# Optimization experiments

Measured on AMD Instinct MI355X. Metric: run time of the kernel, lower is better.

## Reference

```python
import jax, jax.numpy as jnp
import numpy as np

M = 0.4
S = 64.0
EPS = 1e-5

def _normalize(x, axis=-1):
    n = jnp.linalg.norm(x, axis=axis, keepdims=True)
    return x / jnp.maximum(n, EPS)

def setup_inputs() -> dict:
    key = jax.random.key(0)
    k1, k2, k3 = jax.random.split(key, 3)
    B, D, C = 512, 512, 100000
    inp = jax.random.normal(k1, (B, D), dtype=jnp.float32)
    weight = jax.random.normal(k2, (C, D), dtype=jnp.float32) * (D ** -0.5)
    label = jax.random.randint(k3, (B,), 0, C, dtype=jnp.int64)
    bias = jnp.full((1,), float(np.log(C * 10)), dtype=jnp.float32)
    return {"input": inp, "label": label, "weight": weight, "bias": bias}

def reference(input, label, weight, bias):
    # cos_theta: [B, C]
    cos_theta = _normalize(input) @ _normalize(weight).T
    cos_m_theta_p = S * (cos_theta - M) - bias
    cos_m_theta_n = S * cos_theta - bias
    # log(1 + exp(x)) with clamp to [-S, S] as in the original
    p_loss = jnp.log1p(jnp.exp(-jnp.clip(cos_m_theta_p, -S, S)))
    n_loss = jnp.log1p(jnp.exp(jnp.clip(cos_m_theta_n, -S, S)))
    one_hot = jax.nn.one_hot(label, cos_theta.shape[1], dtype=jnp.bool_)
    losses = jnp.where(one_hot, p_loss, n_loss)
    return losses.sum(axis=1).mean()
```

## Files before the change

### kernel.cpp

```cpp
#include <hip/hip_runtime.h>
#include <hip/hip_bf16.h>
#include <stdint.h>

#define C_CLS  100000
#define DDIM   512
#define BROWS  512
#define NT     64
#define KC     32
#define NSTEP  (DDIM / KC)
#define EPSN   1e-5f

typedef __attribute__((ext_vector_type(8))) short short8;
typedef __attribute__((ext_vector_type(4))) float f32x4;

__device__ inline unsigned f2bf(float f) {
  unsigned u = __float_as_uint(f);
  u += 0x7fffu + ((u >> 16) & 1u);
  return u >> 16;
}

__global__ void k_zero(float* acc) { *acc = 0.f; }

__global__ void __launch_bounds__(64) k_norm_input(const float* __restrict__ in,
                                                   uint4* __restrict__ xnf) {
  int b = blockIdx.x;
  int lane = threadIdx.x;
  const float4* row = (const float4*)(in + b * DDIM);
  float4 v0 = row[lane * 2];
  float4 v1 = row[lane * 2 + 1];
  float ss = v0.x*v0.x + v0.y*v0.y + v0.z*v0.z + v0.w*v0.w
           + v1.x*v1.x + v1.y*v1.y + v1.z*v1.z + v1.w*v1.w;
#pragma unroll
  for (int o = 32; o >= 1; o >>= 1) ss += __shfl_xor(ss, o, 64);
  float sc = 1.f / fmaxf(sqrtf(ss), EPSN);
  uint4 o4;
  o4.x = f2bf(v0.x*sc) | (f2bf(v0.y*sc) << 16);
  o4.y = f2bf(v0.z*sc) | (f2bf(v0.w*sc) << 16);
  o4.z = f2bf(v1.x*sc) | (f2bf(v1.y*sc) << 16);
  o4.w = f2bf(v1.z*sc) | (f2bf(v1.w*sc) << 16);
  int idx = ((b >> 4) * 16 + (lane >> 2)) * 64 + (lane & 3) * 16 + (b & 15);
  xnf[idx] = o4;
}

__global__ void __launch_bounds__(512, 4) k_gemm(const uint4* __restrict__ xnf,
                                                 const float* __restrict__ wt,
                                                 const float* __restrict__ bias,
                                                 float* __restrict__ acc_out) {
  __shared__ __align__(16) unsigned char sW[4][4096];
  __shared__ float sNsq[NT];
  __shared__ float sRed[8];

  const int tid  = threadIdx.x;
  const int lane = tid & 63;
  const int wv   = tid >> 6;
  const int cbase = blockIdx.x * NT;

  const int cls = tid >> 3;
  const int q   = tid & 7;
  int wcls = cbase + cls;
  if (wcls >= C_CLS) wcls = C_CLS - 1;
  const float4* wsrc = (const float4*)(wt + (size_t)wcls * DDIM) + q;
  const int wbyte = ((cls >> 4) * 64 + (q >> 1) * 16 + (cls & 15)) * 16 + (q & 1) * 8;

  float wsq = 0.f;
  f32x4 acc[4][4];
#pragma unroll
  for (int m = 0; m < 4; m++)
#pragma unroll
    for (int n = 0; n < 4; n++) acc[m][n] = (f32x4)(0.f);

  auto cvt_write = [&](const float4& w, int bufi) {
    wsq += w.x*w.x + w.y*w.y + w.z*w.z + w.w*w.w;
    uint2 d;
    d.x = f2bf(w.x) | (f2bf(w.y) << 16);
    d.y = f2bf(w.z) | (f2bf(w.w) << 16);
    *(uint2*)(&sW[bufi][wbyte]) = d;
  };
  auto barrier = [&]() {
    __builtin_amdgcn_sched_barrier(0);
    asm volatile("s_waitcnt lgkmcnt(0)" ::: "memory");
    __builtin_amdgcn_s_barrier();
    __builtin_amdgcn_sched_barrier(0);
  };
  auto do_step = [&](int s, float4& wcur, float4& wnext) {
    short8 af[4];
#pragma unroll
    for (int m = 0; m < 4; m++) {
      int idx = ((wv * 4 + m) * 16 + s) * 64 + lane;
      af[m] = *(const short8*)&xnf[idx];
    }
    if (s + 2 < NSTEP) wnext = wsrc[(s + 2) * 8];
    if (s + 1 < NSTEP) cvt_write(wcur, (s + 1) & 3);
    barrier();
    const unsigned char* Wb = sW[s & 3];
#pragma unroll
    for (int n = 0; n < 4; n++) {
      short8 wf = *(const short8*)(Wb + (n * 64 + lane) * 16);
#pragma unroll
      for (int m = 0; m < 4; m++)
        acc[m][n] = __builtin_amdgcn_mfma_f32_16x16x32_bf16(af[m], wf, acc[m][n], 0, 0, 0);
    }
  };

  float4 wA = wsrc[0];
  float4 wB = wsrc[8];
  cvt_write(wA, 0);
  barrier();

#pragma unroll 1
  for (int s = 0; s < NSTEP; s += 2) {
    do_step(s,     wB, wA);
    do_step(s + 1, wA, wB);
  }

#pragma unroll
  for (int o = 1; o < 8; o <<= 1) wsq += __shfl_xor(wsq, o, 64);
  if ((tid & 7) == 0) sNsq[cls] = wsq;
  __syncthreads();

  const float bv = bias[0];
  float sum = 0.f;
#pragma unroll
  for (int n = 0; n < 4; n++) {
    int cl = n * 16 + (lane & 15);
    float rn = 1.f / fmaxf(sqrtf(sNsq[cl]), EPSN);
    bool valid = (cbase + cl) < C_CLS;
#pragma unroll
    for (int m = 0; m < 4; m++) {
#pragma unroll
      for (int i = 0; i < 4; i++) {
        float cosv = acc[m][n][i] * rn;
        float x = fminf(fmaf(cosv, 64.f, -bv), 64.f);
        float z = __expf(x);
        float l = z * fmaf(z, fmaf(z, 0.33333333f, -0.5f), 1.f);
        if (z > 0.03125f) l = __logf(1.f + z);
        sum += valid ? l : 0.f;
      }
    }
  }
#pragma unroll
  for (int o = 32; o >= 1; o >>= 1) sum += __shfl_xor(sum, o, 64);
  if (lane == 0) sRed[wv] = sum;
  __syncthreads();
  if (tid == 0) {
    float t = 0.f;
#pragma unroll
    for (int i = 0; i < 8; i++) t += sRed[i];
    atomicAdd(acc_out, t);
  }
}

__global__ void __launch_bounds__(64) k_label(const float* __restrict__ in,
                                              const float* __restrict__ wt,
                                              const int* __restrict__ label,
                                              const float* __restrict__ bias,
                                              float* __restrict__ acc_out) {
  int b = blockIdx.x;
  int lane = threadIdx.x;
  int c = label[b];
  const float4* xr = (const float4*)(in + b * DDIM);
  const float4* wr = (const float4*)(wt + (size_t)c * DDIM);
  float dt = 0.f, sx = 0.f, sw = 0.f;
#pragma unroll
  for (int i = 0; i < 2; i++) {
    float4 x = xr[lane * 2 + i];
    float4 w = wr[lane * 2 + i];
    dt += x.x*w.x + x.y*w.y + x.z*w.z + x.w*w.w;
    sx += x.x*x.x + x.y*x.y + x.z*x.z + x.w*x.w;
    sw += w.x*w.x + w.y*w.y + w.z*w.z + w.w*w.w;
  }
#pragma unroll
  for (int o = 32; o >= 1; o >>= 1) {
    dt += __shfl_xor(dt, o, 64);
    sx += __shfl_xor(sx, o, 64);
    sw += __shfl_xor(sw, o, 64);
  }
  if (lane == 0) {
    float bv = bias[0];
    float cosv = dt / (fmaxf(sqrtf(sx), EPSN) * fmaxf(sqrtf(sw), EPSN));
    float cp = 64.f * (cosv - 0.4f) - bv;
    cp = fminf(fmaxf(cp, -64.f), 64.f);
    float pl = log1pf(expf(-cp));
    float cn = 64.f * cosv - bv;
    cn = fminf(fmaxf(cn, -64.f), 64.f);
    float nl = log1pf(expf(cn));
    atomicAdd(acc_out, pl - nl);
  }
}

__global__ void k_final(const float* acc, float* out) { out[0] = acc[0] * (1.f / 512.f); }

extern "C" void kernel_launch(void* const* d_in, const int* in_sizes, int n_in,
                              void* d_out, int out_size, void* d_ws, size_t ws_size,
                              hipStream_t stream) {
  const float* input  = (const float*)d_in[0];
  const int*   label  = (const int*)d_in[1];
  const float* weight = (const float*)d_in[2];
  const float* bias   = (const float*)d_in[3];

  float* acc = (float*)d_ws;
  uint4* xnf = (uint4*)((char*)d_ws + 256);

  k_zero<<<1, 1, 0, stream>>>(acc);
  k_norm_input<<<BROWS, 64, 0, stream>>>(input, xnf);
  k_gemm<<<(C_CLS + NT - 1) / NT, 512, 0, stream>>>(xnf, weight, bias, acc);
  k_label<<<BROWS, 64, 0, stream>>>(input, weight, label, bias, acc);
  k_final<<<1, 1, 0, stream>>>(acc, (float*)d_out);
}
```

Before: 116.1 us.

## Restructure GEMM pipeline with prefetched A fragments, swizzled LDS, fewer launches

The main GEMM loop is restructured so the next step's A fragments and the W tile for three steps ahead are prefetched, with the barrier moved to the end of each step and the loop fully unrolled. Shared-memory W writes and reads get an XOR swizzle to reduce bank conflicts, and the normalized-input layout is reordered so A loads become contiguous per step. The zero and final kernels are removed by zeroing the output inside the norm kernel and scaling each atomic contribution by 1/512. bf16 packing now uses the HIP intrinsic. The extra prefetch buffers raise register pressure under launch bounds of 512 threads with 4 blocks.

```diff
diff --git a/kernel.cpp b/kernel.cpp
--- a/kernel.cpp
+++ b/kernel.cpp
@@ -6,25 +6,23 @@
 #define DDIM   512
 #define BROWS  512
 #define NT     64
-#define KC     32
-#define NSTEP  (DDIM / KC)
+#define NSTEP  16
 #define EPSN   1e-5f
 
 typedef __attribute__((ext_vector_type(8))) short short8;
 typedef __attribute__((ext_vector_type(4))) float f32x4;
 
-__device__ inline unsigned f2bf(float f) {
-  unsigned u = __float_as_uint(f);
-  u += 0x7fffu + ((u >> 16) & 1u);
-  return u >> 16;
-}
-
-__global__ void k_zero(float* acc) { *acc = 0.f; }
+__device__ inline unsigned pk2(float a, float b) {
+  __hip_bfloat162 h = __float22bfloat162_rn(make_float2(a, b));
+  unsigned u; __builtin_memcpy(&u, &h, 4); return u;
+}
 
 __global__ void __launch_bounds__(64) k_norm_input(const float* __restrict__ in,
-                                                   uint4* __restrict__ xnf) {
+                                                   uint4* __restrict__ xnf,
+                                                   float* __restrict__ out) {
   int b = blockIdx.x;
   int lane = threadIdx.x;
+  if (b == 0 && lane == 0) out[0] = 0.f;
   const float4* row = (const float4*)(in + b * DDIM);
   float4 v0 = row[lane * 2];
   float4 v1 = row[lane * 2 + 1];
@@ -34,18 +32,18 @@
   for (int o = 32; o >= 1; o >>= 1) ss += __shfl_xor(ss, o, 64);
   float sc = 1.f / fmaxf(sqrtf(ss), EPSN);
   uint4 o4;
-  o4.x = f2bf(v0.x*sc) | (f2bf(v0.y*sc) << 16);
-  o4.y = f2bf(v0.z*sc) | (f2bf(v0.w*sc) << 16);
-  o4.z = f2bf(v1.x*sc) | (f2bf(v1.y*sc) << 16);
-  o4.w = f2bf(v1.z*sc) | (f2bf(v1.w*sc) << 16);
-  int idx = ((b >> 4) * 16 + (lane >> 2)) * 64 + (lane & 3) * 16 + (b & 15);
+  o4.x = pk2(v0.x*sc, v0.y*sc);
+  o4.y = pk2(v0.z*sc, v0.w*sc);
+  o4.z = pk2(v1.x*sc, v1.y*sc);
+  o4.w = pk2(v1.z*sc, v1.w*sc);
+  int idx = ((lane >> 2) * 32 + (b >> 4)) * 64 + (lane & 3) * 16 + (b & 15);
   xnf[idx] = o4;
 }
 
 __global__ void __launch_bounds__(512, 4) k_gemm(const uint4* __restrict__ xnf,
                                                  const float* __restrict__ wt,
                                                  const float* __restrict__ bias,
-                                                 float* __restrict__ acc_out) {
+                                                 float* __restrict__ out) {
   __shared__ __align__(16) unsigned char sW[4][4096];
   __shared__ float sNsq[NT];
   __shared__ float sRed[8];
@@ -60,7 +58,11 @@
   int wcls = cbase + cls;
   if (wcls >= C_CLS) wcls = C_CLS - 1;
   const float4* wsrc = (const float4*)(wt + (size_t)wcls * DDIM) + q;
-  const int wbyte = ((cls >> 4) * 64 + (q >> 1) * 16 + (cls & 15)) * 16 + (q & 1) * 8;
+  const int wcell = (cls >> 4) * 64 + (q >> 1) * 16 + (cls & 15);
+  const int wbyte = ((wcell * 16) ^ (((wcell >> 4) & 3) << 4)) + (q & 1) * 8;
+  const int rbyte = (lane * 16) ^ (((lane >> 4) & 3) << 4);
+
+  const uint4* abase = xnf + wv * 256 + lane;
 
   float wsq = 0.f;
   f32x4 acc[4][4];
@@ -69,11 +71,16 @@
 #pragma unroll
     for (int n = 0; n < 4; n++) acc[m][n] = (f32x4)(0.f);
 
+  auto loadA = [&](short8* af, int s) {
+#pragma unroll
+    for (int m = 0; m < 4; m++)
+      af[m] = *(const short8*)(abase + s * 2048 + m * 64);
+  };
   auto cvt_write = [&](const float4& w, int bufi) {
     wsq += w.x*w.x + w.y*w.y + w.z*w.z + w.w*w.w;
     uint2 d;
-    d.x = f2bf(w.x) | (f2bf(w.y) << 16);
-    d.y = f2bf(w.z) | (f2bf(w.w) << 16);
+    d.x = pk2(w.x, w.y);
+    d.y = pk2(w.z, w.w);
     *(uint2*)(&sW[bufi][wbyte]) = d;
   };
   auto barrier = [&]() {
@@ -82,35 +89,33 @@
     __builtin_amdgcn_s_barrier();
     __builtin_amdgcn_sched_barrier(0);
   };
-  auto do_step = [&](int s, float4& wcur, float4& wnext) {
-    short8 af[4];
-#pragma unroll
-    for (int m = 0; m < 4; m++) {
-      int idx = ((wv * 4 + m) * 16 + s) * 64 + lane;
-      af[m] = *(const short8*)&xnf[idx];
+  auto step = [&](int s, float4& wreg, short8* afc, short8* afn) {
+    if (s + 1 < NSTEP) loadA(afn, s + 1);
+    if (s + 1 < NSTEP) cvt_write(wreg, (s + 1) & 3);
+    if (s + 3 < NSTEP) wreg = wsrc[(s + 3) * 8];
+    const unsigned char* Wb = sW[s & 3];
+#pragma unroll
+    for (int n = 0; n < 4; n++) {
+      short8 wf = *(const short8*)(Wb + n * 1024 + rbyte);
+#pragma unroll
+      for (int m = 0; m < 4; m++)
+        acc[m][n] = __builtin_amdgcn_mfma_f32_16x16x32_bf16(afc[m], wf, acc[m][n], 0, 0, 0);
     }
-    if (s + 2 < NSTEP) wnext = wsrc[(s + 2) * 8];
-    if (s + 1 < NSTEP) cvt_write(wcur, (s + 1) & 3);
-    barrier();
-    const unsigned char* Wb = sW[s & 3];
-#pragma unroll
-    for (int n = 0; n < 4; n++) {
-      short8 wf = *(const short8*)(Wb + (n * 64 + lane) * 16);
-#pragma unroll
-      for (int m = 0; m < 4; m++)
-        acc[m][n] = __builtin_amdgcn_mfma_f32_16x16x32_bf16(af[m], wf, acc[m][n], 0, 0, 0);
-    }
-  };
-
-  float4 wA = wsrc[0];
-  float4 wB = wsrc[8];
-  cvt_write(wA, 0);
+    if (s + 1 < NSTEP) barrier();
+  };
+
+  short8 af0[4], af1[4];
+  loadA(af0, 0);
+  float4 w0 = wsrc[0];
+  float4 wA = wsrc[8];
+  float4 wB = wsrc[16];
+  cvt_write(w0, 0);
   barrier();
 
-#pragma unroll 1
-  for (int s = 0; s < NSTEP; s += 2) {
-    do_step(s,     wB, wA);
-    do_step(s + 1, wA, wB);
+#pragma unroll
+  for (int s = 0; s < NSTEP; s++) {
+    if (s & 1) step(s, wB, af1, af0);
+    else       step(s, wA, af0, af1);
   }
 
 #pragma unroll
@@ -146,7 +151,7 @@
     float t = 0.f;
 #pragma unroll
     for (int i = 0; i < 8; i++) t += sRed[i];
-    atomicAdd(acc_out, t);
+    atomicAdd(out, t * (1.f / 512.f));
   }
 }
 
@@ -154,7 +159,7 @@
                                               const float* __restrict__ wt,
                                               const int* __restrict__ label,
                                               const float* __restrict__ bias,
-                                              float* __restrict__ acc_out) {
+                                              float* __restrict__ out) {
   int b = blockIdx.x;
   int lane = threadIdx.x;
   int c = label[b];
@@ -184,11 +189,9 @@
     float cn = 64.f * cosv - bv;
     cn = fminf(fmaxf(cn, -64.f), 64.f);
     float nl = log1pf(expf(cn));
-    atomicAdd(acc_out, pl - nl);
-  }
-}
-
-__global__ void k_final(const float* acc, float* out) { out[0] = acc[0] * (1.f / 512.f); }
+    atomicAdd(out, (pl - nl) * (1.f / 512.f));
+  }
+}
 
 extern "C" void kernel_launch(void* const* d_in, const int* in_sizes, int n_in,
                               void* d_out, int out_size, void* d_ws, size_t ws_size,
@@ -197,13 +200,11 @@
   const int*   label  = (const int*)d_in[1];
   const float* weight = (const float*)d_in[2];
   const float* bias   = (const float*)d_in[3];
-
-  float* acc = (float*)d_ws;
-  uint4* xnf = (uint4*)((char*)d_ws + 256);
-
-  k_zero<<<1, 1, 0, stream>>>(acc);
-  k_norm_input<<<BROWS, 64, 0, stream>>>(input, xnf);
-  k_gemm<<<(C_CLS + NT - 1) / NT, 512, 0, stream>>>(xnf, weight, bias, acc);
-  k_label<<<BROWS, 64, 0, stream>>>(input, weight, label, bias, acc);
-  k_final<<<1, 1, 0, stream>>>(acc, (float*)d_out);
-}
+  float* out = (float*)d_out;
+
+  uint4* xnf = (uint4*)d_ws;
+
+  k_norm_input<<<BROWS, 64, 0, stream>>>(input, xnf, out);
+  k_gemm<<<(C_CLS + NT - 1) / NT, 512, 0, stream>>>(xnf, weight, bias, out);
+  k_label<<<BROWS, 64, 0, stream>>>(input, weight, label, bias, out);
+}
```

Result: slower. 200.3 us (+72.5%).
